# Kernel tuning notes

Hardware: AMD Instinct MI355X
Metric: run time of the kernel (lower is better)

The kernel has to match this reference:

```python
import jax, jax.numpy as jnp
import numpy as np

B, S, VOCAB, HID, NCLS = 64, 512, 1400, 256, 128


def _time_lstm(W_all, b_all, U_all, b_u, W_d, b_d, x, ts):
    # x: [b, s, h], ts: [b, s]
    b = x.shape[0]
    h0 = jnp.zeros((b, HID), x.dtype)
    c0 = jnp.zeros((b, HID), x.dtype)

    def step(carry, xt):
        h, c = carry
        x_t, t_t = xt  # [b,h], [b]
        c_s1 = jnp.tanh(c @ W_d.T + b_d)
        c_adj = (c - c_s1) + c_s1 * t_t[:, None]
        gates = jax.nn.sigmoid(h @ W_all.T + b_all + x_t @ U_all.T + b_u)
        f, i, o, c_tmp = jnp.split(gates, 4, axis=1)  # note: c_tmp is sigmoid, as in source
        c_new = f * c_adj + i * c_tmp
        h_new = o * jnp.tanh(c_new)
        return (h_new, c_new), h_new

    _, hs = jax.lax.scan(step, (h0, c0), (x.transpose(1, 0, 2), ts.T))
    return hs.transpose(1, 0, 2)  # [b, s, h]


def setup_inputs() -> dict:
    key = jax.random.key(0)
    ks = jax.random.split(key, 18)

    def g(k, shape, scale=0.05):
        return jax.random.normal(k, shape, dtype=jnp.float32) * scale

    return {
        "inputs": jax.random.uniform(ks[0], (B, S, VOCAB), dtype=jnp.float32),
        "timestamps": jax.random.uniform(ks[1], (B, S), dtype=jnp.float32),
        "emb": g(ks[2], (VOCAB, HID)),
        "W_all1": g(ks[3], (4 * HID, HID)), "b_all1": g(ks[4], (4 * HID,)),
        "U_all1": g(ks[5], (4 * HID, HID)), "b_u1": g(ks[6], (4 * HID,)),
        "W_d1": g(ks[7], (HID, HID)), "b_d1": g(ks[8], (HID,)),
        "W_all2": g(ks[9], (4 * HID, HID)), "b_all2": g(ks[10], (4 * HID,)),
        "U_all2": g(ks[11], (4 * HID, HID)), "b_u2": g(ks[12], (4 * HID,)),
        "W_d2": g(ks[13], (HID, HID)), "b_d2": g(ks[14], (HID,)),
        "wa": g(ks[15], (1, HID)),
        "Wb": g(ks[16], (HID, HID)),
        "W_out": g(ks[17], (NCLS, HID)),
    }


def reference(inputs, timestamps, emb, W_all1, b_all1, U_all1, b_u1, W_d1, b_d1,
              W_all2, b_all2, U_all2, b_u2, W_d2, b_d2, wa, Wb, W_out):
    embedded = jnp.einsum('bsv,vh->bsh', inputs, emb)  # multi-hot embedding lookup
    out1 = _time_lstm(W_all1, b_all1, U_all1, b_u1, W_d1, b_d1, embedded, timestamps)
    out2 = _time_lstm(W_all2, b_all2, U_all2, b_u2, W_d2, b_d2, embedded, timestamps)
    alpha = jax.nn.softmax(jnp.einsum('bsh,oh->bs', out1, wa), axis=1)  # [b,s]
    Beta = jnp.tanh(jnp.einsum('bsh,gh->bsg', out2, Wb))  # [b,s,h]
    ctx = jnp.sum(embedded * Beta * alpha[:, :, None], axis=1)  # [b,h]
    return ctx @ W_out.T  # [b, num_classes]
```

## Files before the change

kernel.cpp:

```cpp
#include <hip/hip_runtime.h>

typedef __attribute__((ext_vector_type(8))) short short8;
typedef __attribute__((ext_vector_type(4))) float f32x4;

#define B_   64
#define S_   512
#define V_   1400
#define VP_  1408
#define H_   256
#define G4_  1024
#define NC_  128
#define CH_  64

__device__ __forceinline__ unsigned short f2bf(float f) {
    unsigned u = __builtin_bit_cast(unsigned, f);
    u += 0x7FFFu + ((u >> 16) & 1u);
    return (unsigned short)(u >> 16);
}
__device__ __forceinline__ float bf2f(unsigned short h) {
    unsigned u = ((unsigned)h) << 16;
    return __builtin_bit_cast(float, u);
}
__device__ __forceinline__ float fsig(float x) {
    x = fminf(fmaxf(x, -40.f), 40.f);
    float e = __builtin_amdgcn_exp2f(x * -1.44269504f);
    return __builtin_amdgcn_rcpf(1.0f + e);
}
__device__ __forceinline__ float ftanh(float x) {
    x = fminf(fmaxf(x, -40.f), 40.f);
    float e = __builtin_amdgcn_exp2f(x * 2.88539008f);
    return 1.0f - 2.0f * __builtin_amdgcn_rcpf(e + 1.0f);
}

__device__ __forceinline__ short8 gload16_sc1(const unsigned short* p) {
    short8 r;
    asm volatile("global_load_dwordx4 %0, %1, off sc1"
                 : "=&v"(r) : "v"((unsigned long long)p));
    return r;
}
__device__ __forceinline__ void gstore_short_sc1(unsigned short* p, unsigned v) {
    asm volatile("global_store_short %0, %1, off sc1"
                 :: "v"((unsigned long long)p), "v"(v));
}
__device__ __forceinline__ short8 gload16_sc0(const unsigned short* p) {
    short8 r;
    asm volatile("global_load_dwordx4 %0, %1, off sc0"
                 : "=&v"(r) : "v"((unsigned long long)p));
    return r;
}
__device__ __forceinline__ void gstore_short_plain(unsigned short* p, unsigned v) {
    asm volatile("global_store_short %0, %1, off"
                 :: "v"((unsigned long long)p), "v"(v));
}

#define CNT_ZONE_ 6144

__global__ void k0_prep(const float* __restrict__ emb,
                        const float* __restrict__ Wa1, const float* __restrict__ Wa2,
                        const float* __restrict__ Wd1, const float* __restrict__ Wd2,
                        const float* __restrict__ U1,  const float* __restrict__ U2,
                        const float* __restrict__ ba1, const float* __restrict__ bu1,
                        const float* __restrict__ ba2, const float* __restrict__ bu2,
                        const float* __restrict__ Wb,
                        unsigned short* __restrict__ embT, unsigned short* __restrict__ Wg,
                        unsigned short* __restrict__ Wd,   unsigned short* __restrict__ Ub,
                        unsigned short* __restrict__ Wbb,  float* __restrict__ bg,
                        unsigned int* __restrict__ cnt) {
    int tid = blockIdx.x * blockDim.x + threadIdx.x;
    int np = gridDim.x * blockDim.x;
    for (int i = tid; i < 256 * VP_; i += np) {
        int n = i / VP_, k = i - n * VP_;
        embT[i] = (k < V_) ? f2bf(emb[k * H_ + n]) : (unsigned short)0;
    }
    for (int i = tid; i < G4_ * H_; i += np) {
        Wg[i] = f2bf(Wa1[i]); Wg[G4_ * H_ + i] = f2bf(Wa2[i]);
        Ub[i] = f2bf(U1[i]);  Ub[G4_ * H_ + i] = f2bf(U2[i]);
    }
    for (int i = tid; i < H_ * H_; i += np) {
        Wd[i] = f2bf(Wd1[i]); Wd[H_ * H_ + i] = f2bf(Wd2[i]); Wbb[i] = f2bf(Wb[i]);
    }
    for (int i = tid; i < G4_; i += np) {
        bg[i] = ba1[i] + bu1[i]; bg[G4_ + i] = ba2[i] + bu2[i];
    }
    for (int i = tid; i < CNT_ZONE_; i += np) cnt[i] = 0;
}

__global__ __launch_bounds__(512, 2) void k1_embed(const float* __restrict__ inputs,
                                                   const unsigned short* __restrict__ embT,
                                                   unsigned short* __restrict__ embB) {
    const int tid = threadIdx.x;
    const int w = tid >> 6, ln = tid & 63, q = ln >> 4, l16 = ln & 15;
    const int mt = w >> 2, ng = (w & 3) * 4;
    const int Rbase = blockIdx.x * 32 + mt * 16;
    const float* arow = inputs + (long)(Rbase + l16) * V_;

    f32x4 acc[4];
    #pragma unroll
    for (int i = 0; i < 4; ++i) acc[i] = (f32x4){0.f, 0.f, 0.f, 0.f};

    for (int kt = 0; kt < 44; ++kt) {
        int k0 = kt * 32 + q * 8;
        short8 af;
        if (kt == 43 && q == 3) {
            #pragma unroll
            for (int j = 0; j < 8; ++j) af[j] = 0;
        } else {
            f32x4 x0 = *(const f32x4*)(arow + k0);
            f32x4 x1 = *(const f32x4*)(arow + k0 + 4);
            #pragma unroll
            for (int j = 0; j < 4; ++j) { af[j] = (short)f2bf(x0[j]); af[4 + j] = (short)f2bf(x1[j]); }
        }
        #pragma unroll
        for (int i = 0; i < 4; ++i) {
            short8 bf = *(const short8*)(embT + (long)((ng + i) * 16 + l16) * VP_ + k0);
            acc[i] = __builtin_amdgcn_mfma_f32_16x16x32_bf16(af, bf, acc[i], 0, 0, 0);
        }
    }
    #pragma unroll
    for (int i = 0; i < 4; ++i) {
        int col = (ng + i) * 16 + l16;
        #pragma unroll
        for (int j = 0; j < 4; ++j) {
            int R = Rbase + 4 * q + j;
            embB[(long)R * H_ + col] = f2bf(acc[i][j]);
        }
    }
}

__global__ __launch_bounds__(512, 2) void k2_pre(const unsigned short* __restrict__ embB,
                                                 const unsigned short* __restrict__ Ub,
                                                 const float* __restrict__ bg,
                                                 float* __restrict__ P, int t0) {
    const int tid = threadIdx.x;
    const int w = tid >> 6, ln = tid & 63, q = ln >> 4, l16 = ln & 15;
    const int rbase = blockIdx.x * 32;

    short8 af[2][8];
    #pragma unroll
    for (int mt = 0; mt < 2; ++mt)
        #pragma unroll
        for (int kt = 0; kt < 8; ++kt) {
            int rp = rbase + mt * 16 + l16;
            int rg = t0 * 64 + rp;
            int b = rg & 63, s = rg >> 6;
            af[mt][kt] = *(const short8*)(embB + ((long)b * S_ + s) * H_ + kt * 32 + q * 8);
        }

    for (int i = 0; i < 16; ++i) {
        int nt2 = w * 16 + i;
        int l = nt2 >> 6;
        int gcol = (nt2 & 63) * 16 + l16;
        float bias = bg[nt2 * 16 + l16];
        short8 bf[8];
        #pragma unroll
        for (int kt = 0; kt < 8; ++kt)
            bf[kt] = *(const short8*)(Ub + (long)(nt2 * 16 + l16) * H_ + kt * 32 + q * 8);
        #pragma unroll
        for (int mt = 0; mt < 2; ++mt) {
            f32x4 acc = (f32x4){bias, bias, bias, bias};
            #pragma unroll
            for (int kt = 0; kt < 8; ++kt)
                acc = __builtin_amdgcn_mfma_f32_16x16x32_bf16(af[mt][kt], bf[kt], acc, 0, 0, 0);
            int rp0 = rbase + mt * 16;
            float* dst = P + ((long)l * (CH_ * 64) + rp0 + 4 * q) * G4_ + gcol;
            #pragma unroll
            for (int j = 0; j < 4; ++j) dst[(long)j * G4_] = acc[j];
        }
    }
}

__global__ __launch_bounds__(256, 1) void k3_lstm(const float* __restrict__ ts,
                                                  const unsigned short* __restrict__ W,
                                                  const float* __restrict__ bd1,
                                                  const float* __restrict__ bd2,
                                                  const float* __restrict__ P,
                                                  unsigned short* __restrict__ out1,
                                                  unsigned short* __restrict__ out2,
                                                  float* __restrict__ cst,
                                                  unsigned short* __restrict__ cx,
                                                  unsigned int* __restrict__ cnt,
                                                  int t0) {
    __shared__ float ts_lds[16][CH_];

    const int tid = threadIdx.x;
    const int w = tid >> 6, ln = tid & 63, q = ln >> 4, l16 = ln & 15;
    const int bid = blockIdx.x;
    const int chunk = t0 >> 6;

    const int myx = (int)__builtin_amdgcn_s_getreg(63508);
    unsigned int* rdy  = cnt + 4096 + chunk * 64;
    int*          xpub = (int*)(cnt + 4608);
    if (tid == 0) {
        __hip_atomic_store(&xpub[bid], myx, __ATOMIC_RELAXED, __HIP_MEMORY_SCOPE_AGENT);
        __hip_atomic_fetch_add(rdy, 1u, __ATOMIC_RELEASE, __HIP_MEMORY_SCOPE_AGENT);
    }
    unsigned hs_it = 0;
    while (__hip_atomic_load(rdy, __ATOMIC_ACQUIRE, __HIP_MEMORY_SCOPE_AGENT) < 32u
           && ++hs_it < (1u << 20))
        __builtin_amdgcn_s_sleep(2);
    int xv[32];
    #pragma unroll
    for (int i = 0; i < 32; ++i)
        xv[i] = __hip_atomic_load(&xpub[i], __ATOMIC_RELAXED, __HIP_MEMORY_SCOPE_AGENT);
    unsigned okA = 1, inr = 1, mask = 0;
    #pragma unroll
    for (int g = 0; g < 8; ++g)
        okA &= (unsigned)((xv[g] == xv[g + 8]) & (xv[g] == xv[g + 16]) & (xv[g] == xv[g + 24]));
    #pragma unroll
    for (int i = 0; i < 32; ++i) {
        inr &= (unsigned)((unsigned)xv[i] < 8u);
        mask |= 1u << ((unsigned)xv[i] & 31u);
    }
    const bool fast = okA && inr && (mask == 0xFFu) && (hs_it < (1u << 20));

    const int grp = bid & 7, cg = bid >> 3;
    const int l = grp >> 2, m = grp & 3, b0 = m * 16;
    const int hc0 = cg * 64 + w * 16;
    const int mycol = hc0 + l16;
    unsigned int* cell = cnt + (chunk * 8 + grp) * 64;
    unsigned short* outp = l ? out2 : out1;
    const float bdv = (l ? bd2 : bd1)[mycol];

    for (int i = tid; i < 16 * CH_; i += 256) {
        int r = i >> 6, cc = i & (CH_ - 1);
        ts_lds[r][cc] = ts[(b0 + r) * S_ + t0 + cc];
    }

    short8 wg[4][8];
    short8 wd[8];
    #pragma unroll
    for (int g = 0; g < 4; ++g)
        #pragma unroll
        for (int kt = 0; kt < 8; ++kt)
            wg[g][kt] = *(const short8*)(W + ((long)(l * G4_ + g * H_ + mycol)) * H_ + kt * 32 + q * 8);
    #pragma unroll
    for (int kt = 0; kt < 8; ++kt)
        wd[kt] = *(const short8*)(W + (long)2 * G4_ * H_ + ((long)(l * H_ + mycol)) * H_ + kt * 32 + q * 8);

    float cf[4];
    if (t0 == 0) {
        cf[0] = cf[1] = cf[2] = cf[3] = 0.f;
    } else {
        #pragma unroll
        for (int j = 0; j < 4; ++j)
            cf[j] = cst[(long)(l * 4 + m) * 4096 + (4 * q + j) * 256 + mycol];
    }
    __syncthreads();

    const float* Pbase = P + ((long)l * (CH_ * 64) + b0) * G4_;

    if (fast) {
        unsigned opaque_zero;
        asm volatile("v_mov_b32 %0, 0" : "=v"(opaque_zero));

        float pv[4][4];
        #pragma unroll
        for (int g = 0; g < 4; ++g)
            #pragma unroll
            for (int j = 0; j < 4; ++j)
                pv[g][j] = Pbase[((long)(4 * q + j)) * G4_ + g * H_ + mycol];
        asm volatile("" ::: "memory");

        #pragma unroll 1
        for (int t = 0; t < CH_; ++t) {
            const int gt = t0 + t;

            if (t) {
                const unsigned tgt = 16u * (unsigned)t;
                unsigned it = 0;
                for (;;) {
                    unsigned v = 0;
                    if (ln == 0)
                        v = __hip_atomic_fetch_add(cell, opaque_zero,
                                                   __ATOMIC_RELAXED, __HIP_MEMORY_SCOPE_WORKGROUP);
                    v = __shfl(v, 0);
                    if (v >= tgt || ++it >= (1u << 14)) break;
                }
            }
            __builtin_amdgcn_fence(__ATOMIC_ACQUIRE, "agent");
            __builtin_amdgcn_sched_barrier(0);

            short8 ha[8], ca[8];
            if (gt == 0) {
                #pragma unroll
                for (int kt = 0; kt < 8; ++kt) {
                    #pragma unroll
                    for (int j = 0; j < 8; ++j) { ha[kt][j] = 0; ca[kt][j] = 0; }
                }
            } else {
                const unsigned short* crow = cx + ((long)(((gt - 1) & 1) * 8 + grp)) * 4096 + l16 * 256 + q * 8;
                const unsigned short* hrow = outp + ((long)(b0 + l16) * S_ + (gt - 1)) * H_ + q * 8;
                #pragma unroll
                for (int kt = 0; kt < 8; ++kt) ca[kt] = gload16_sc0(crow + kt * 32);
                #pragma unroll
                for (int kt = 0; kt < 8; ++kt) ha[kt] = gload16_sc0(hrow + kt * 32);
            }
            asm volatile("s_waitcnt vmcnt(8)" ::: "memory");
            __builtin_amdgcn_sched_barrier(0);

            f32x4 dacc = (f32x4){bdv, bdv, bdv, bdv};
            #pragma unroll
            for (int kt = 0; kt < 8; ++kt)
                dacc = __builtin_amdgcn_mfma_f32_16x16x32_bf16(ca[kt], wd[kt], dacc, 0, 0, 0);

            asm volatile("s_waitcnt vmcnt(0)" ::: "memory");
            __builtin_amdgcn_sched_barrier(0);

            f32x4 gacc[4];
            #pragma unroll
            for (int g = 0; g < 4; ++g) {
                gacc[g] = (f32x4){pv[g][0], pv[g][1], pv[g][2], pv[g][3]};
                #pragma unroll
                for (int kt = 0; kt < 8; ++kt)
                    gacc[g] = __builtin_amdgcn_mfma_f32_16x16x32_bf16(ha[kt], wg[g][kt], gacc[g], 0, 0, 0);
            }

            #pragma unroll
            for (int j = 0; j < 4; ++j) {
                int r = 4 * q + j;
                float tv = ts_lds[r][t];
                float cs1 = ftanh(dacc[j]);
                float cadj = cf[j] + cs1 * (tv - 1.0f);
                float fg = fsig(gacc[0][j]), ig = fsig(gacc[1][j]);
                float og = fsig(gacc[2][j]), ct = fsig(gacc[3][j]);
                float cn = fg * cadj + ig * ct;
                float hn = og * ftanh(cn);
                cf[j] = cn;
                gstore_short_plain(outp + ((long)(b0 + r) * S_ + gt) * H_ + mycol, (unsigned)f2bf(hn));
                gstore_short_plain(cx + ((long)((gt & 1) * 8 + grp)) * 4096 + r * 256 + mycol, (unsigned)f2bf(cn));
            }
            asm volatile("s_waitcnt vmcnt(0)" ::: "memory");
            if (ln == 0)
                __hip_atomic_fetch_add(cell, 1u, __ATOMIC_RELAXED, __HIP_MEMORY_SCOPE_WORKGROUP);

            {
                int tn = (t + 1 < CH_) ? t + 1 : t;
                asm volatile("" ::: "memory");
                #pragma unroll
                for (int g = 0; g < 4; ++g)
                    #pragma unroll
                    for (int j = 0; j < 4; ++j)
                        pv[g][j] = Pbase[((long)tn * 64 + 4 * q + j) * G4_ + g * H_ + mycol];
                asm volatile("" ::: "memory");
            }
        }
    } else {
        #pragma unroll 1
        for (int t = 0; t < CH_; ++t) {
            const int gt = t0 + t;

            float pv[4][4];
            #pragma unroll
            for (int g = 0; g < 4; ++g)
                #pragma unroll
                for (int j = 0; j < 4; ++j)
                    pv[g][j] = Pbase[((long)t * 64 + 4 * q + j) * G4_ + g * H_ + mycol];
            asm volatile("" ::: "memory");

            {
                unsigned tgt = 4u * (unsigned)t, it = 0;
                while (__hip_atomic_load(cell, __ATOMIC_RELAXED, __HIP_MEMORY_SCOPE_AGENT) < tgt
                       && ++it < (1u << 18))
                    __builtin_amdgcn_s_sleep(1);
            }

            short8 ha[8], ca[8];
            if (gt == 0) {
                #pragma unroll
                for (int kt = 0; kt < 8; ++kt) {
                    #pragma unroll
                    for (int j = 0; j < 8; ++j) { ha[kt][j] = 0; ca[kt][j] = 0; }
                }
            } else {
                const unsigned short* crow = cx + ((long)(((gt - 1) & 1) * 8 + grp)) * 4096 + l16 * 256 + q * 8;
                const unsigned short* hrow = outp + ((long)(b0 + l16) * S_ + (gt - 1)) * H_ + q * 8;
                #pragma unroll
                for (int kt = 0; kt < 8; ++kt) ca[kt] = gload16_sc1(crow + kt * 32);
                #pragma unroll
                for (int kt = 0; kt < 8; ++kt) ha[kt] = gload16_sc1(hrow + kt * 32);
            }
            asm volatile("s_waitcnt vmcnt(8)" ::: "memory");
            __builtin_amdgcn_sched_barrier(0);

            f32x4 dacc = (f32x4){bdv, bdv, bdv, bdv};
            #pragma unroll
            for (int kt = 0; kt < 8; ++kt)
                dacc = __builtin_amdgcn_mfma_f32_16x16x32_bf16(ca[kt], wd[kt], dacc, 0, 0, 0);

            asm volatile("s_waitcnt vmcnt(0)" ::: "memory");
            __builtin_amdgcn_sched_barrier(0);

            f32x4 gacc[4];
            #pragma unroll
            for (int g = 0; g < 4; ++g) {
                gacc[g] = (f32x4){pv[g][0], pv[g][1], pv[g][2], pv[g][3]};
                #pragma unroll
                for (int kt = 0; kt < 8; ++kt)
                    gacc[g] = __builtin_amdgcn_mfma_f32_16x16x32_bf16(ha[kt], wg[g][kt], gacc[g], 0, 0, 0);
            }

            #pragma unroll
            for (int j = 0; j < 4; ++j) {
                int r = 4 * q + j;
                float tv = ts_lds[r][t];
                float cs1 = ftanh(dacc[j]);
                float cadj = cf[j] + cs1 * (tv - 1.0f);
                float fg = fsig(gacc[0][j]), ig = fsig(gacc[1][j]);
                float og = fsig(gacc[2][j]), ct = fsig(gacc[3][j]);
                float cn = fg * cadj + ig * ct;
                float hn = og * ftanh(cn);
                cf[j] = cn;
                gstore_short_sc1(outp + ((long)(b0 + r) * S_ + gt) * H_ + mycol, (unsigned)f2bf(hn));
                gstore_short_sc1(cx + ((long)((gt & 1) * 8 + grp)) * 4096 + r * 256 + mycol, (unsigned)f2bf(cn));
            }
            asm volatile("s_waitcnt vmcnt(0)" ::: "memory");
            __syncthreads();
            if (tid == 0) atomicAdd(cell, 1u);
        }
    }

    #pragma unroll
    for (int j = 0; j < 4; ++j)
        cst[(long)(l * 4 + m) * 4096 + (4 * q + j) * 256 + mycol] = cf[j];
}

__global__ __launch_bounds__(512) void k4a_alpha(const unsigned short* __restrict__ out1,
                                                 const float* __restrict__ wa,
                                                 float* __restrict__ alpha) {
    __shared__ float sc[512];
    __shared__ float red[512];
    const int b = blockIdx.x, tid = threadIdx.x;
    const int w = tid >> 6, ln = tid & 63;
    f32x4 wv = *(const f32x4*)(wa + ln * 4);
    for (int i = 0; i < 64; ++i) {
        int s = w * 64 + i;
        const unsigned short* row = out1 + ((long)b * S_ + s) * H_ + ln * 4;
        float d = bf2f(row[0]) * wv[0] + bf2f(row[1]) * wv[1] +
                  bf2f(row[2]) * wv[2] + bf2f(row[3]) * wv[3];
        #pragma unroll
        for (int off = 32; off; off >>= 1) d += __shfl_xor(d, off);
        if (ln == 0) sc[s] = d;
    }
    __syncthreads();
    float v = sc[tid];
    red[tid] = v;
    for (int st = 256; st; st >>= 1) {
        __syncthreads();
        if (tid < st) red[tid] = fmaxf(red[tid], red[tid + st]);
    }
    __syncthreads();
    float M = red[0];
    __syncthreads();
    float e = __builtin_amdgcn_exp2f((v - M) * 1.44269504f);
    red[tid] = e;
    for (int st = 256; st; st >>= 1) {
        __syncthreads();
        if (tid < st) red[tid] += red[tid + st];
    }
    __syncthreads();
    alpha[b * S_ + tid] = e * __builtin_amdgcn_rcpf(red[0]);
}

__global__ __launch_bounds__(512, 2) void k4b_ctx(const unsigned short* __restrict__ out2,
                                                  const unsigned short* __restrict__ Wbb,
                                                  const unsigned short* __restrict__ embB,
                                                  const float* __restrict__ alpha,
                                                  float* __restrict__ ctx) {
    __shared__ float cbuf[32][256];
    const int b = blockIdx.x, tid = threadIdx.x;
    const int w = tid >> 6, ln = tid & 63, q = ln >> 4, l16 = ln & 15;

    float cp[16];
    #pragma unroll
    for (int nt = 0; nt < 16; ++nt) cp[nt] = 0.f;

    for (int i = 0; i < 4; ++i) {
        int mt = w * 4 + i;
        short8 af[8];
        #pragma unroll
        for (int kt = 0; kt < 8; ++kt)
            af[kt] = *(const short8*)(out2 + ((long)b * S_ + mt * 16 + l16) * H_ + kt * 32 + q * 8);
        float al[4];
        #pragma unroll
        for (int j = 0; j < 4; ++j) al[j] = alpha[b * S_ + mt * 16 + 4 * q + j];
        for (int nt = 0; nt < 16; ++nt) {
            f32x4 acc = (f32x4){0.f, 0.f, 0.f, 0.f};
            #pragma unroll
            for (int kt = 0; kt < 8; ++kt) {
                short8 bf = *(const short8*)(Wbb + (long)(nt * 16 + l16) * H_ + kt * 32 + q * 8);
                acc = __builtin_amdgcn_mfma_f32_16x16x32_bf16(af[kt], bf, acc, 0, 0, 0);
            }
            #pragma unroll
            for (int j = 0; j < 4; ++j) {
                int s = mt * 16 + 4 * q + j;
                float beta = ftanh(acc[j]);
                float ev = bf2f(embB[((long)b * S_ + s) * H_ + nt * 16 + l16]);
                cp[nt] += beta * al[j] * ev;
            }
        }
    }
    #pragma unroll
    for (int nt = 0; nt < 16; ++nt) cbuf[w * 4 + q][nt * 16 + l16] = cp[nt];
    __syncthreads();
    if (tid < 256) {
        float sum = 0.f;
        for (int i = 0; i < 32; ++i) sum += cbuf[i][tid];
        ctx[b * H_ + tid] = sum;
    }
}

__global__ void k4c_out(const float* __restrict__ ctx, const float* __restrict__ Wout,
                        float* __restrict__ out) {
    int b = blockIdx.x, n = threadIdx.x;
    const f32x4* cr = (const f32x4*)(ctx + b * H_);
    const f32x4* wr = (const f32x4*)(Wout + n * H_);
    float acc = 0.f;
    #pragma unroll 8
    for (int i = 0; i < 64; ++i) {
        f32x4 c = cr[i], ww = wr[i];
        acc += c[0] * ww[0] + c[1] * ww[1] + c[2] * ww[2] + c[3] * ww[3];
    }
    out[b * NC_ + n] = acc;
}

extern "C" void kernel_launch(void* const* d_in, const int* in_sizes, int n_in,
                              void* d_out, int out_size, void* d_ws, size_t ws_size,
                              hipStream_t stream) {
    (void)in_sizes; (void)n_in; (void)out_size; (void)ws_size;
    const float* inputs = (const float*)d_in[0];
    const float* tsp    = (const float*)d_in[1];
    const float* emb    = (const float*)d_in[2];
    const float* Wa1 = (const float*)d_in[3];  const float* ba1 = (const float*)d_in[4];
    const float* U1  = (const float*)d_in[5];  const float* bu1 = (const float*)d_in[6];
    const float* Wd1 = (const float*)d_in[7];  const float* bd1 = (const float*)d_in[8];
    const float* Wa2 = (const float*)d_in[9];  const float* ba2 = (const float*)d_in[10];
    const float* U2  = (const float*)d_in[11]; const float* bu2 = (const float*)d_in[12];
    const float* Wd2 = (const float*)d_in[13]; const float* bd2 = (const float*)d_in[14];
    const float* wa  = (const float*)d_in[15];
    const float* Wb  = (const float*)d_in[16];
    const float* Wout = (const float*)d_in[17];
    float* out = (float*)d_out;

    char* ws = (char*)d_ws;
    unsigned short* embT = (unsigned short*)(ws + 0);
    unsigned short* Wg   = (unsigned short*)(ws + 720896);
    unsigned short* Wd   = (unsigned short*)(ws + 1769472);
    unsigned short* Ub   = (unsigned short*)(ws + 2031616);
    unsigned short* Wbb  = (unsigned short*)(ws + 3080192);
    float*          bgp  = (float*)(ws + 3211264);
    unsigned short* embB = (unsigned short*)(ws + 3219456);
    float*          P    = (float*)(ws + 19996672);
    unsigned short* out1 = (unsigned short*)(ws + 53551104);
    unsigned short* out2 = (unsigned short*)(ws + 70328320);
    unsigned short* cx   = (unsigned short*)(ws + 87105536);
    float*          cst  = (float*)(ws + 87236608);
    float*          alp  = (float*)(ws + 87367680);
    float*          ctx  = (float*)(ws + 87498752);
    unsigned int*   cnt  = (unsigned int*)(ws + 87564288);

    hipLaunchKernelGGL(k0_prep, dim3(256), dim3(256), 0, stream,
                       emb, Wa1, Wa2, Wd1, Wd2, U1, U2, ba1, bu1, ba2, bu2, Wb,
                       embT, Wg, Wd, Ub, Wbb, bgp, cnt);
    hipLaunchKernelGGL(k1_embed, dim3(1024), dim3(512), 0, stream, inputs, embT, embB);
    for (int c = 0; c < 8; ++c) {
        hipLaunchKernelGGL(k2_pre, dim3(128), dim3(512), 0, stream, embB, Ub, bgp, P, c * CH_);
        hipLaunchKernelGGL(k3_lstm, dim3(32), dim3(256), 0, stream, tsp, Wg, bd1, bd2, P,
                           out1, out2, cst, cx, cnt, c * CH_);
    }
    hipLaunchKernelGGL(k4a_alpha, dim3(64), dim3(512), 0, stream, out1, wa, alp);
    hipLaunchKernelGGL(k4b_ctx, dim3(64), dim3(512), 0, stream, out2, Wbb, embB, alp, ctx);
    hipLaunchKernelGGL(k4c_out, dim3(64), dim3(128), 0, stream, ctx, Wout, out);
}
```

Baseline: 3.077 ms.

## Overlap next-chunk input projection with LSTM recurrence and add per-step flag polling

Fuses the k2_pre input-projection GEMM for the next time chunk into the recurrent LSTM kernel as extra blocks, double-buffering the P projection buffer so chunk c+1's precompute runs alongside chunk c's recurrence. It also adds per-step per-wave flag words that are polled with plain vector loads before falling back to the atomic counter spin. The intent is to hide the projection GEMM and the launch gaps behind the latency-bound 32-block recurrence and to cut atomic polling latency. It needs a larger workspace, falls back to the old path when the workspace is too small, and the extra blocks may compete for memory bandwidth or CUs with the recurrence.

```diff
diff --git a/kernel.cpp b/kernel.cpp
--- a/kernel.cpp
+++ b/kernel.cpp
@@ -2,6 +2,7 @@
 
 typedef __attribute__((ext_vector_type(8))) short short8;
 typedef __attribute__((ext_vector_type(4))) float f32x4;
+typedef __attribute__((ext_vector_type(4))) unsigned int u32x4;
 
 #define B_   64
 #define S_   512
@@ -52,8 +53,23 @@
     asm volatile("global_store_short %0, %1, off"
                  :: "v"((unsigned long long)p), "v"(v));
 }
-
-#define CNT_ZONE_ 6144
+__device__ __forceinline__ void gstore_dword_plain(unsigned int* p, unsigned v) {
+    asm volatile("global_store_dword %0, %1, off"
+                 :: "v"((unsigned long long)p), "v"(v));
+}
+__device__ __forceinline__ void gpoll16_plain(const unsigned int* p,
+                                              u32x4& f0, u32x4& f1, u32x4& f2, u32x4& f3) {
+    asm volatile("global_load_dwordx4 %0, %4, off\n\t"
+                 "global_load_dwordx4 %1, %5, off\n\t"
+                 "global_load_dwordx4 %2, %6, off\n\t"
+                 "global_load_dwordx4 %3, %7, off\n\t"
+                 "s_waitcnt vmcnt(0)"
+                 : "=&v"(f0), "=&v"(f1), "=&v"(f2), "=&v"(f3)
+                 : "v"((unsigned long long)p),        "v"((unsigned long long)(p + 4)),
+                   "v"((unsigned long long)(p + 8)),  "v"((unsigned long long)(p + 12)));
+}
+
+#define CNT_ZONE_ 38912
 
 __global__ void k0_prep(const float* __restrict__ emb,
                         const float* __restrict__ Wa1, const float* __restrict__ Wa2,
@@ -169,22 +185,67 @@
     }
 }
 
-__global__ __launch_bounds__(256, 1) void k3_lstm(const float* __restrict__ ts,
-                                                  const unsigned short* __restrict__ W,
-                                                  const float* __restrict__ bd1,
-                                                  const float* __restrict__ bd2,
-                                                  const float* __restrict__ P,
-                                                  unsigned short* __restrict__ out1,
-                                                  unsigned short* __restrict__ out2,
-                                                  float* __restrict__ cst,
-                                                  unsigned short* __restrict__ cx,
-                                                  unsigned int* __restrict__ cnt,
-                                                  int t0) {
-    __shared__ float ts_lds[16][CH_];
-
+__global__ __launch_bounds__(256, 1) void k3_fused(const float* __restrict__ ts,
+                                                   const unsigned short* __restrict__ W,
+                                                   const float* __restrict__ bd1,
+                                                   const float* __restrict__ bd2,
+                                                   const float* __restrict__ Pcur,
+                                                   unsigned short* __restrict__ out1,
+                                                   unsigned short* __restrict__ out2,
+                                                   float* __restrict__ cst,
+                                                   unsigned short* __restrict__ cx,
+                                                   unsigned int* __restrict__ cnt,
+                                                   int t0,
+                                                   const unsigned short* __restrict__ embB,
+                                                   const unsigned short* __restrict__ Ub,
+                                                   const float* __restrict__ bg,
+                                                   float* __restrict__ Pnext,
+                                                   int next_t0) {
     const int tid = threadIdx.x;
     const int w = tid >> 6, ln = tid & 63, q = ln >> 4, l16 = ln & 15;
     const int bid = blockIdx.x;
+
+    if (bid >= 32) {
+        const int g2 = bid - 32;
+        const int rbase = (g2 >> 1) * 32;
+        const int hb = g2 & 1;
+
+        short8 af[2][8];
+        #pragma unroll
+        for (int mt = 0; mt < 2; ++mt)
+            #pragma unroll
+            for (int kt = 0; kt < 8; ++kt) {
+                int rp = rbase + mt * 16 + l16;
+                int rg = next_t0 * 64 + rp;
+                int b = rg & 63, s = rg >> 6;
+                af[mt][kt] = *(const short8*)(embB + ((long)b * S_ + s) * H_ + kt * 32 + q * 8);
+            }
+
+        for (int i = 0; i < 16; ++i) {
+            int nt2 = hb * 64 + w * 16 + i;
+            int l = nt2 >> 6;
+            int gcol = (nt2 & 63) * 16 + l16;
+            float bias = bg[nt2 * 16 + l16];
+            short8 bf[8];
+            #pragma unroll
+            for (int kt = 0; kt < 8; ++kt)
+                bf[kt] = *(const short8*)(Ub + (long)(nt2 * 16 + l16) * H_ + kt * 32 + q * 8);
+            #pragma unroll
+            for (int mt = 0; mt < 2; ++mt) {
+                f32x4 acc = (f32x4){bias, bias, bias, bias};
+                #pragma unroll
+                for (int kt = 0; kt < 8; ++kt)
+                    acc = __builtin_amdgcn_mfma_f32_16x16x32_bf16(af[mt][kt], bf[kt], acc, 0, 0, 0);
+                int rp0 = rbase + mt * 16;
+                float* dst = Pnext + ((long)l * (CH_ * 64) + rp0 + 4 * q) * G4_ + gcol;
+                #pragma unroll
+                for (int j = 0; j < 4; ++j) dst[(long)j * G4_] = acc[j];
+            }
+        }
+        return;
+    }
+
+    __shared__ float ts_lds[16][CH_];
     const int chunk = t0 >> 6;
 
     const int myx = (int)__builtin_amdgcn_s_getreg(63508);
@@ -218,6 +279,7 @@
     const int hc0 = cg * 64 + w * 16;
     const int mycol = hc0 + l16;
     unsigned int* cell = cnt + (chunk * 8 + grp) * 64;
+    unsigned int* fbase = cnt + 6144 + (long)chunk * 64 * 64;
     unsigned short* outp = l ? out2 : out1;
     const float bdv = (l ? bd2 : bd1)[mycol];
 
@@ -247,7 +309,7 @@
     }
     __syncthreads();
 
-    const float* Pbase = P + ((long)l * (CH_ * 64) + b0) * G4_;
+    const float* Pbase = Pcur + ((long)l * (CH_ * 64) + b0) * G4_;
 
     if (fast) {
         unsigned opaque_zero;
@@ -266,15 +328,23 @@
             const int gt = t0 + t;
 
             if (t) {
-                const unsigned tgt = 16u * (unsigned)t;
-                unsigned it = 0;
-                for (;;) {
-                    unsigned v = 0;
-                    if (ln == 0)
-                        v = __hip_atomic_fetch_add(cell, opaque_zero,
-                                                   __ATOMIC_RELAXED, __HIP_MEMORY_SCOPE_WORKGROUP);
-                    v = __shfl(v, 0);
-                    if (v >= tgt || ++it >= (1u << 14)) break;
+                const unsigned int* fprev = fbase + (long)(t - 1) * 64;
+                u32x4 f0, f1, f2, f3;
+                gpoll16_plain(fprev, f0, f1, f2, f3);
+                unsigned s = 0;
+                #pragma unroll
+                for (int i = 0; i < 4; ++i) s += f0[i] + f1[i] + f2[i] + f3[i];
+                if (s != 16u) {
+                    const unsigned tgt = 16u * (unsigned)t;
+                    unsigned it = 0;
+                    for (;;) {
+                        unsigned v = 0;
+                        if (ln == 0)
+                            v = __hip_atomic_fetch_add(cell, opaque_zero,
+                                                       __ATOMIC_RELAXED, __HIP_MEMORY_SCOPE_WORKGROUP);
+                        v = __shfl(v, 0);
+                        if (v >= tgt || ++it >= (1u << 14)) break;
+                    }
                 }
             }
             __builtin_amdgcn_fence(__ATOMIC_ACQUIRE, "agent");
@@ -330,8 +400,10 @@
                 gstore_short_plain(cx + ((long)((gt & 1) * 8 + grp)) * 4096 + r * 256 + mycol, (unsigned)f2bf(cn));
             }
             asm volatile("s_waitcnt vmcnt(0)" ::: "memory");
-            if (ln == 0)
-                __hip_atomic_fetch_add(cell, 1u, __ATOMIC_RELAXED, __HIP_MEMORY_SCOPE_WORKGROUP);
+            if (ln == 0) {
+                gstore_dword_plain(fbase + (long)t * 64 + (cg * 4 + w), 1u);
+                (void)__hip_atomic_fetch_add(cell, 1u, __ATOMIC_RELAXED, __HIP_MEMORY_SCOPE_WORKGROUP);
+            }
 
             {
                 int tn = (t + 1 < CH_) ? t + 1 : t;
@@ -526,7 +598,7 @@
 extern "C" void kernel_launch(void* const* d_in, const int* in_sizes, int n_in,
                               void* d_out, int out_size, void* d_ws, size_t ws_size,
                               hipStream_t stream) {
-    (void)in_sizes; (void)n_in; (void)out_size; (void)ws_size;
+    (void)in_sizes; (void)n_in; (void)out_size;
     const float* inputs = (const float*)d_in[0];
     const float* tsp    = (const float*)d_in[1];
     const float* emb    = (const float*)d_in[2];
@@ -549,7 +621,7 @@
     unsigned short* Wbb  = (unsigned short*)(ws + 3080192);
     float*          bgp  = (float*)(ws + 3211264);
     unsigned short* embB = (unsigned short*)(ws + 3219456);
-    float*          P    = (float*)(ws + 19996672);
+    float*          P0   = (float*)(ws + 19996672);
     unsigned short* out1 = (unsigned short*)(ws + 53551104);
     unsigned short* out2 = (unsigned short*)(ws + 70328320);
     unsigned short* cx   = (unsigned short*)(ws + 87105536);
@@ -557,15 +629,30 @@
     float*          alp  = (float*)(ws + 87367680);
     float*          ctx  = (float*)(ws + 87498752);
     unsigned int*   cnt  = (unsigned int*)(ws + 87564288);
+    float*          P1   = (float*)(ws + 87719936);
+    const size_t NEED_FUSED = 121274368;
+    const bool fuse = (ws_size >= NEED_FUSED);
 
     hipLaunchKernelGGL(k0_prep, dim3(256), dim3(256), 0, stream,
                        emb, Wa1, Wa2, Wd1, Wd2, U1, U2, ba1, bu1, ba2, bu2, Wb,
                        embT, Wg, Wd, Ub, Wbb, bgp, cnt);
     hipLaunchKernelGGL(k1_embed, dim3(1024), dim3(512), 0, stream, inputs, embT, embB);
+    hipLaunchKernelGGL(k2_pre, dim3(128), dim3(512), 0, stream, embB, Ub, bgp, P0, 0);
+
+    float* Pb[2] = { P0, fuse ? P1 : P0 };
     for (int c = 0; c < 8; ++c) {
-        hipLaunchKernelGGL(k2_pre, dim3(128), dim3(512), 0, stream, embB, Ub, bgp, P, c * CH_);
-        hipLaunchKernelGGL(k3_lstm, dim3(32), dim3(256), 0, stream, tsp, Wg, bd1, bd2, P,
-                           out1, out2, cst, cx, cnt, c * CH_);
+        if (fuse) {
+            int ng = (c < 7) ? 256 : 0;
+            hipLaunchKernelGGL(k3_fused, dim3(32 + ng), dim3(256), 0, stream,
+                               tsp, Wg, bd1, bd2, Pb[c & 1], out1, out2, cst, cx, cnt, c * CH_,
+                               embB, Ub, bgp, Pb[(c + 1) & 1], (c + 1) * CH_);
+        } else {
+            if (c > 0)
+                hipLaunchKernelGGL(k2_pre, dim3(128), dim3(512), 0, stream, embB, Ub, bgp, P0, c * CH_);
+            hipLaunchKernelGGL(k3_fused, dim3(32), dim3(256), 0, stream,
+                               tsp, Wg, bd1, bd2, P0, out1, out2, cst, cx, cnt, c * CH_,
+                               embB, Ub, bgp, P0, S_ );
+        }
     }
     hipLaunchKernelGGL(k4a_alpha, dim3(64), dim3(512), 0, stream, out1, wa, alp);
     hipLaunchKernelGGL(k4b_ctx, dim3(64), dim3(512), 0, stream, out2, Wbb, embB, alp, ctx);
```

After: 2.822 ms. 1.09x faster.
